# Kernel tuning notes

Hardware: AMD Instinct MI355X
Metric: run time of the kernel (lower is better)

## Reference

```python
import jax, jax.numpy as jnp
import numpy as np

NH = 256   # nh_rnn
V = 21     # joints
TC = 60    # cont time dim
CC = 4     # cont channels
DCT_N = 60
T_HIS = 30
HORIZON = 60
BS = 256


def _lin(x, w, b):
    # torch nn.Linear convention: w is [out, in]
    return x @ w.T + b


def setup_inputs() -> dict:
    key = jax.random.key(0)
    ks = iter(jax.random.split(key, 48))

    def rn(shape, s=1.0):
        return jax.random.normal(next(ks), shape, dtype=jnp.float32) * jnp.float32(s)

    inp = {}
    inp["x"] = rn((T_HIS, BS, 63))
    inp["cont"] = rn((BS, TC, V * CC))
    inp["cont_mask"] = jnp.ones((BS, TC), jnp.float32)  # never used (per docstring)
    inp["dct_m"] = rn((DCT_N, T_HIS + HORIZON), 0.1)
    inp["idct_m"] = rn((T_HIS + HORIZON, DCT_N), 0.1)
    inp["root_idx"] = jnp.array([42, 43, 44], dtype=jnp.int32)
    inp["horizon"] = HORIZON

    # --- STSGCN_layer(cont): learned temporal/spatial adjacencies + 1x1 convs + BN(folded) + PReLU ---
    inp["T_c"] = rn((V, TC, TC), 1.0 / np.sqrt(TC))
    inp["A_c"] = rn((TC, V, V), 1.0 / np.sqrt(V))
    inp["conv_w"] = rn((NH, CC), 0.5)
    inp["conv_b"] = rn((NH,), 0.1)
    inp["bn1_scale"] = 1.0 + rn((NH,), 0.1)
    inp["bn1_shift"] = rn((NH,), 0.1)
    inp["resconv_w"] = rn((NH, CC), 0.5)
    inp["resconv_b"] = rn((NH,), 0.1)
    inp["bnr_scale"] = 1.0 + rn((NH,), 0.1)
    inp["bnr_shift"] = rn((NH,), 0.1)
    inp["prelu_a"] = jnp.float32(0.25)

    # tiny MLP encoders
    inp["te1_w"] = rn((10, TC), 1.0 / np.sqrt(TC)); inp["te1_b"] = rn((10,), 0.1)
    inp["te2_w"] = rn((1, 10), 1.0 / np.sqrt(10)); inp["te2_b"] = rn((1,), 0.1)
    inp["ne1_w"] = rn((10, V), 1.0 / np.sqrt(V)); inp["ne1_b"] = rn((10,), 0.1)
    inp["ne2_w"] = rn((1, 10), 1.0 / np.sqrt(10)); inp["ne2_b"] = rn((1,), 0.1)

    # residual MLP head
    din = DCT_N * 3 + NH
    inp["g1_w"] = rn((NH, din), 1.0 / np.sqrt(din)); inp["g1_b"] = rn((NH,), 0.1)
    inp["g2a_w"] = rn((NH, NH), 1.0 / np.sqrt(NH)); inp["g2a_b"] = rn((NH,), 0.1)
    inp["g2b_w"] = rn((NH, NH), 1.0 / np.sqrt(NH)); inp["g2b_b"] = rn((NH,), 0.1)
    inp["g3a_w"] = rn((NH, NH), 1.0 / np.sqrt(NH)); inp["g3a_b"] = rn((NH,), 0.1)
    inp["g3b_w"] = rn((NH, NH), 1.0 / np.sqrt(NH)); inp["g3b_b"] = rn((NH,), 0.1)
    inp["g4_w"] = rn((DCT_N * 3, NH), 1.0 / np.sqrt(NH)); inp["g4_b"] = rn((DCT_N * 3,), 0.1)
    return inp


def reference(x, cont, cont_mask, dct_m, idct_m, root_idx, horizon,
              T_c, A_c, conv_w, conv_b, bn1_scale, bn1_shift,
              resconv_w, resconv_b, bnr_scale, bnr_shift, prelu_a,
              te1_w, te1_b, te2_w, te2_b, ne1_w, ne1_b, ne2_w, ne2_b,
              g1_w, g1_b, g2a_w, g2a_b, g2b_w, g2b_b,
              g3a_w, g3a_b, g3b_w, g3b_b, g4_w, g4_b):
    t_his, bs, _ = x.shape

    # --- root history padded with last frame, then batched DCT ---
    pad_idx = jnp.concatenate([jnp.arange(t_his), jnp.full((horizon,), t_his - 1)])
    root_his = x[:, :, root_idx][pad_idx].transpose(1, 0, 2)                 # [bs, 90, 3]
    root_his_dct = jnp.einsum('dt,btk->bdk', dct_m, root_his).reshape(bs, -1)  # [bs, 180]

    # --- STSGCN layer on contact stream: [b, 4, 60, 21] ---
    xc = cont.reshape(bs, TC, V, CC).transpose(0, 3, 1, 2)                   # [b,c,t,v]
    res = jnp.einsum('nctv,oc->notv', xc, resconv_w) + resconv_b[None, :, None, None]
    res = res * bnr_scale[None, :, None, None] + bnr_shift[None, :, None, None]
    g = jnp.einsum('nctv,vtq->ncqv', xc, T_c)    # temporal adjacency
    g = jnp.einsum('nctv,tvw->nctw', g, A_c)     # spatial adjacency
    h = jnp.einsum('nctv,oc->notv', g, conv_w) + conv_b[None, :, None, None]
    h = h * bn1_scale[None, :, None, None] + bn1_shift[None, :, None, None]
    h = h + res
    h = jnp.where(h >= 0, h, prelu_a * h)        # PReLU, [b, 256, 60, 21]

    # --- time encoder: collapse t=60 -> 1 ---
    ht = h.transpose(0, 1, 3, 2).reshape(bs, NH * V, TC)
    ht = jnp.tanh(_lin(jnp.tanh(_lin(ht, te1_w, te1_b)), te2_w, te2_b))[..., 0]
    # --- node encoder: collapse v=21 -> 1 ---
    hn = ht.reshape(bs, NH, V)
    hcont = jnp.tanh(_lin(jnp.tanh(_lin(hn, ne1_w, ne1_b)), ne2_w, ne2_b))[..., 0]  # [bs, 256]

    # --- residual MLP head on DCT coefficients ---
    rh = jnp.tanh(_lin(jnp.concatenate([root_his_dct, hcont], axis=1), g1_w, g1_b))
    rh = jnp.tanh(_lin(jnp.tanh(_lin(rh, g2a_w, g2a_b)), g2b_w, g2b_b)) + rh
    rh = jnp.tanh(_lin(jnp.tanh(_lin(rh, g3a_w, g3a_b)), g3b_w, g3b_b)) + rh
    root_pred = _lin(rh, g4_w, g4_b) + root_his_dct                          # [bs, 180]
    root_traj = jnp.einsum('td,bdk->btk', idct_m, root_pred.reshape(bs, DCT_N, 3))
    return root_traj                                                          # [bs, 90, 3]
```

## Files before the change

### kernel.cpp

```cpp
#include <hip/hip_runtime.h>

#define NHID 256
#define NV   21
#define NT   60
#define NC   4
#define NDCT 60
#define THIS 30
#define NBS  256

__device__ __forceinline__ float ftanh(float x) {
    float e = __expf(2.0f * x);
    return 1.0f - __fdividef(2.0f, e + 1.0f);
}

__global__ __launch_bounds__(512, 2) void k_main(
    const float* __restrict__ cont,
    const float* __restrict__ T_c, const float* __restrict__ A_c,
    const float* __restrict__ conv_w, const float* __restrict__ conv_b,
    const float* __restrict__ bn1_scale, const float* __restrict__ bn1_shift,
    const float* __restrict__ resconv_w, const float* __restrict__ resconv_b,
    const float* __restrict__ bnr_scale, const float* __restrict__ bnr_shift,
    const float* __restrict__ prelu_a_p,
    const float* __restrict__ te1_w, const float* __restrict__ te1_b,
    const float* __restrict__ te2_w, const float* __restrict__ te2_b,
    const float* __restrict__ ne1_w, const float* __restrict__ ne1_b,
    const float* __restrict__ ne2_w, const float* __restrict__ ne2_b,
    float* __restrict__ hcont)
{
    __shared__ __align__(16) float xc_lds[5040];
    __shared__ __align__(16) float g_lds[5040];
    __shared__ __align__(16) float g2_lds[5040];

    const int n   = blockIdx.x;
    const int tid = threadIdx.x;

    {
        const float4* src = (const float4*)(cont + n * 5040);
        float4* dst = (float4*)xc_lds;
        for (int i = tid; i < 1260; i += 512) dst[i] = src[i];
    }
    __syncthreads();

    for (int task = tid; task < 630; task += 512) {
        int v  = task / 30;
        int q0 = (task - v * 30) * 2;
        const float* tc = T_c + v * 3600 + q0;
        float4 a0 = {0.f,0.f,0.f,0.f}, a1 = {0.f,0.f,0.f,0.f};
        #pragma unroll 4
        for (int t = 0; t < 60; ++t) {
            float4 xcv = *(const float4*)(xc_lds + t * 84 + v * 4);
            float2 tq  = *(const float2*)(tc + t * 60);
            a0.x += xcv.x * tq.x; a0.y += xcv.y * tq.x;
            a0.z += xcv.z * tq.x; a0.w += xcv.w * tq.x;
            a1.x += xcv.x * tq.y; a1.y += xcv.y * tq.y;
            a1.z += xcv.z * tq.y; a1.w += xcv.w * tq.y;
        }
        *(float4*)(g_lds + q0 * 84 + v * 4)       = a0;
        *(float4*)(g_lds + (q0 + 1) * 84 + v * 4) = a1;
    }
    __syncthreads();

    for (int task = tid; task < 660; task += 512) {
        int t  = task / 11;
        int w0 = (task - t * 11) * 2;
        const bool has2 = (w0 < 20);
        const float* ac = A_c + t * 441 + w0;
        float4 a0 = {0.f,0.f,0.f,0.f}, a1 = {0.f,0.f,0.f,0.f};
        #pragma unroll
        for (int v = 0; v < 21; ++v) {
            float4 gv = *(const float4*)(g_lds + t * 84 + v * 4);
            float b0 = ac[v * 21];
            float b1 = has2 ? ac[v * 21 + 1] : 0.f;
            a0.x += gv.x * b0; a0.y += gv.y * b0;
            a0.z += gv.z * b0; a0.w += gv.w * b0;
            a1.x += gv.x * b1; a1.y += gv.y * b1;
            a1.z += gv.z * b1; a1.w += gv.w * b1;
        }
        *(float4*)(g2_lds + t * 84 + w0 * 4) = a0;
        if (has2) *(float4*)(g2_lds + t * 84 + (w0 + 1) * 4) = a1;
    }
    __syncthreads();

    const int og = tid >> 3;
    const int part = tid & 7;
    const int vstart = (part < 5) ? part * 3 : 15 + (part - 5) * 2;
    const int vcount = (part < 5) ? 3 : 2;

    const float pa = prelu_a_p[0];

    float cA[4][4], cB[4][4], cC[4];
    #pragma unroll
    for (int g = 0; g < 4; ++g) {
        int o = og * 4 + g;
        float s1 = bn1_scale[o], sr = bnr_scale[o];
        #pragma unroll
        for (int c = 0; c < 4; ++c) {
            cA[g][c] = conv_w[o * 4 + c] * s1;
            cB[g][c] = resconv_w[o * 4 + c] * sr;
        }
        cC[g] = conv_b[o] * s1 + bn1_shift[o] + resconv_b[o] * sr + bnr_shift[o];
    }

    float tw2[10], tb1[10];
    #pragma unroll
    for (int j = 0; j < 10; ++j) { tw2[j] = te2_w[j]; tb1[j] = te1_b[j]; }
    const float tb2 = te2_b[0];

    float wacc[4][10];
    #pragma unroll
    for (int g = 0; g < 4; ++g)
        #pragma unroll
        for (int j = 0; j < 10; ++j) wacc[g][j] = 0.f;

    for (int vi = 0; vi < vcount; ++vi) {
        int v = vstart + vi;
        float u[4][10];
        #pragma unroll
        for (int g = 0; g < 4; ++g)
            #pragma unroll
            for (int j = 0; j < 10; ++j) u[g][j] = tb1[j];

        for (int t = 0; t < 60; ++t) {
            float4 xcv = *(const float4*)(xc_lds + t * 84 + v * 4);
            float4 g2v = *(const float4*)(g2_lds + t * 84 + v * 4);
            float tw[10];
            #pragma unroll
            for (int j = 0; j < 10; ++j) tw[j] = te1_w[j * 60 + t];
            #pragma unroll
            for (int g = 0; g < 4; ++g) {
                float h = cC[g]
                    + cA[g][0] * g2v.x + cA[g][1] * g2v.y + cA[g][2] * g2v.z + cA[g][3] * g2v.w
                    + cB[g][0] * xcv.x + cB[g][1] * xcv.y + cB[g][2] * xcv.z + cB[g][3] * xcv.w;
                h = fmaxf(h, 0.f) + pa * fminf(h, 0.f);
                #pragma unroll
                for (int j = 0; j < 10; ++j) u[g][j] += h * tw[j];
            }
        }

        float nw[10];
        #pragma unroll
        for (int j = 0; j < 10; ++j) nw[j] = ne1_w[j * 21 + v];
        #pragma unroll
        for (int g = 0; g < 4; ++g) {
            float s = tb2;
            #pragma unroll
            for (int j = 0; j < 10; ++j) s += ftanh(u[g][j]) * tw2[j];
            s = ftanh(s);
            #pragma unroll
            for (int j = 0; j < 10; ++j) wacc[g][j] += s * nw[j];
        }
    }

    #pragma unroll
    for (int d = 1; d < 8; d <<= 1)
        #pragma unroll
        for (int g = 0; g < 4; ++g)
            #pragma unroll
            for (int j = 0; j < 10; ++j)
                wacc[g][j] += __shfl_xor(wacc[g][j], d, 64);

    if (part == 0) {
        float nw2[10];
        #pragma unroll
        for (int j = 0; j < 10; ++j) nw2[j] = ne2_w[j];
        float nb2 = ne2_b[0];
        #pragma unroll
        for (int g = 0; g < 4; ++g) {
            int o = og * 4 + g;
            float s = nb2;
            #pragma unroll
            for (int j = 0; j < 10; ++j)
                s += ftanh(wacc[g][j] + ne1_b[j]) * nw2[j];
            hcont[n * 256 + o] = ftanh(s);
        }
    }
}

__global__ __launch_bounds__(512) void k_head(
    const float* __restrict__ x, const float* __restrict__ dct_m,
    const int* __restrict__ root_idx, const float* __restrict__ hcont,
    const float* __restrict__ g1_w, const float* __restrict__ g1_b,
    const float* __restrict__ g2a_w, const float* __restrict__ g2a_b,
    const float* __restrict__ g2b_w, const float* __restrict__ g2b_b,
    const float* __restrict__ g3a_w, const float* __restrict__ g3a_b,
    const float* __restrict__ g3b_w, const float* __restrict__ g3b_b,
    const float* __restrict__ g4_w, const float* __restrict__ g4_b,
    const float* __restrict__ idct_m, float* __restrict__ out)
{
    __shared__ __align__(16) float in_lds[2 * 436];
    __shared__ __align__(16) float a_lds[2 * 256];
    __shared__ __align__(16) float b_lds[2 * 256];
    __shared__ __align__(16) float rp_lds[2 * 180];

    const int tid = threadIdx.x;
    const int n0 = blockIdx.x * 2;
    const int gid = tid >> 3;
    const int sub = tid & 7;

    {
        int bn = tid >> 8, j = tid & 255;
        in_lds[bn * 436 + 180 + j] = hcont[(n0 + bn) * 256 + j];
    }
    for (int i = tid; i < 360; i += 512) {
        int bn = i / 180, r = i - bn * 180;
        int d = r / 3, k = r - d * 3;
        int ri = root_idx[k];
        const float* xp = x + (n0 + bn) * 63 + ri;
        const float* dm = dct_m + d * 90;
        float acc = 0.f;
        #pragma unroll
        for (int t = 0; t < 30; ++t)
            acc += dm[t] * xp[t * 16128];
        float wl = 0.f;
        #pragma unroll
        for (int t = 30; t < 90; ++t)
            wl += dm[t];
        acc += wl * xp[29 * 16128];
        in_lds[bn * 436 + r] = acc;
    }
    __syncthreads();

#define DENSE_CORE(KDIM, NSWEEP, W, SRC, SSTR, GUARD_O, BODY)                   \
    {                                                                           \
        float acc[4][2] = {};                                                   \
        for (int s = 0; s < NSWEEP; ++s) {                                      \
            int k4 = s * 8 + sub;                                               \
            if (k4 * 4 < KDIM) {                                                \
                float4 av0 = *(const float4*)&SRC[0 * SSTR + k4 * 4];           \
                float4 av1 = *(const float4*)&SRC[1 * SSTR + k4 * 4];           \
                _Pragma("unroll")                                               \
                for (int oo = 0; oo < 4; ++oo) {                                \
                    int o = gid * 4 + oo;                                       \
                    if (GUARD_O) {                                              \
                        float4 wv = *(const float4*)&W[o * KDIM + k4 * 4];      \
                        acc[oo][0] += wv.x*av0.x + wv.y*av0.y + wv.z*av0.z + wv.w*av0.w; \
                        acc[oo][1] += wv.x*av1.x + wv.y*av1.y + wv.z*av1.z + wv.w*av1.w; \
                    }                                                           \
                }                                                               \
            }                                                                   \
        }                                                                       \
        _Pragma("unroll")                                                       \
        for (int m = 1; m < 8; m <<= 1) {                                       \
            _Pragma("unroll")                                                   \
            for (int oo = 0; oo < 4; ++oo) {                                    \
                acc[oo][0] += __shfl_xor(acc[oo][0], m, 64);                    \
                acc[oo][1] += __shfl_xor(acc[oo][1], m, 64);                    \
            }                                                                   \
        }                                                                       \
        if (sub == 0) {                                                         \
            _Pragma("unroll")                                                   \
            for (int oo = 0; oo < 4; ++oo) {                                    \
                int o = gid * 4 + oo;                                           \
                if (GUARD_O) {                                                  \
                    _Pragma("unroll")                                           \
                    for (int bn = 0; bn < 2; ++bn) { float sumv = acc[oo][bn]; BODY } \
                }                                                               \
            }                                                                   \
        }                                                                       \
    }                                                                           \
    __syncthreads();

    DENSE_CORE(436, 14, g1_w, in_lds, 436, true,
        { a_lds[bn * 256 + o] = ftanh(sumv + g1_b[o]); })

    DENSE_CORE(256, 8, g2a_w, a_lds, 256, true,
        { b_lds[bn * 256 + o] = ftanh(sumv + g2a_b[o]); })

    DENSE_CORE(256, 8, g2b_w, b_lds, 256, true,
        { a_lds[bn * 256 + o] = ftanh(sumv + g2b_b[o]) + a_lds[bn * 256 + o]; })

    DENSE_CORE(256, 8, g3a_w, a_lds, 256, true,
        { b_lds[bn * 256 + o] = ftanh(sumv + g3a_b[o]); })

    DENSE_CORE(256, 8, g3b_w, b_lds, 256, true,
        { a_lds[bn * 256 + o] = ftanh(sumv + g3b_b[o]) + a_lds[bn * 256 + o]; })

    DENSE_CORE(256, 8, g4_w, a_lds, 256, (o < 180),
        { rp_lds[bn * 180 + o] = sumv + g4_b[o] + in_lds[bn * 436 + o]; })

    for (int idx = tid; idx < 2 * 270; idx += 512) {
        int bn = idx / 270;
        int r = idx - bn * 270;
        int t = r / 3;
        int k = r - t * 3;
        const float* im = idct_m + t * 60;
        const float* rp = rp_lds + bn * 180 + k;
        float acc = 0.f;
        #pragma unroll
        for (int d = 0; d < 60; ++d)
            acc += im[d] * rp[d * 3];
        out[(n0 + bn) * 270 + r] = acc;
    }
}

extern "C" void kernel_launch(void* const* d_in, const int* in_sizes, int n_in,
                              void* d_out, int out_size, void* d_ws, size_t ws_size,
                              hipStream_t stream)
{
    const float* x        = (const float*)d_in[0];
    const float* cont     = (const float*)d_in[1];
    const float* dct_m    = (const float*)d_in[3];
    const float* idct_m   = (const float*)d_in[4];
    const int*   root_idx = (const int*)d_in[5];
    const float* T_c      = (const float*)d_in[7];
    const float* A_c      = (const float*)d_in[8];
    const float* conv_w   = (const float*)d_in[9];
    const float* conv_b   = (const float*)d_in[10];
    const float* bn1_s    = (const float*)d_in[11];
    const float* bn1_sh   = (const float*)d_in[12];
    const float* rconv_w  = (const float*)d_in[13];
    const float* rconv_b  = (const float*)d_in[14];
    const float* bnr_s    = (const float*)d_in[15];
    const float* bnr_sh   = (const float*)d_in[16];
    const float* prelu_a  = (const float*)d_in[17];
    const float* te1_w    = (const float*)d_in[18];
    const float* te1_b    = (const float*)d_in[19];
    const float* te2_w    = (const float*)d_in[20];
    const float* te2_b    = (const float*)d_in[21];
    const float* ne1_w    = (const float*)d_in[22];
    const float* ne1_b    = (const float*)d_in[23];
    const float* ne2_w    = (const float*)d_in[24];
    const float* ne2_b    = (const float*)d_in[25];
    const float* g1_w     = (const float*)d_in[26];
    const float* g1_b     = (const float*)d_in[27];
    const float* g2a_w    = (const float*)d_in[28];
    const float* g2a_b    = (const float*)d_in[29];
    const float* g2b_w    = (const float*)d_in[30];
    const float* g2b_b    = (const float*)d_in[31];
    const float* g3a_w    = (const float*)d_in[32];
    const float* g3a_b    = (const float*)d_in[33];
    const float* g3b_w    = (const float*)d_in[34];
    const float* g3b_b    = (const float*)d_in[35];
    const float* g4_w     = (const float*)d_in[36];
    const float* g4_b     = (const float*)d_in[37];

    float* hcont = (float*)d_ws;

    k_main<<<NBS, 512, 0, stream>>>(cont, T_c, A_c,
                                    conv_w, conv_b, bn1_s, bn1_sh,
                                    rconv_w, rconv_b, bnr_s, bnr_sh,
                                    prelu_a,
                                    te1_w, te1_b, te2_w, te2_b,
                                    ne1_w, ne1_b, ne2_w, ne2_b,
                                    hcont);

    k_head<<<NBS / 2, 512, 0, stream>>>(x, dct_m, root_idx, hcont,
                                        g1_w, g1_b, g2a_w, g2a_b, g2b_w, g2b_b,
                                        g3a_w, g3a_b, g3b_w, g3b_b, g4_w, g4_b,
                                        idct_m, (float*)d_out);
}
```

Baseline: 270.7 us.

## Fuse STSGCN encoder and MLP head into one 1024-thread kernel per sample

Merges the two kernels into a single kernel with one block per batch sample and 1024 threads. Each thread now handles 2 output channels in the encoder instead of 4, and the MLP head runs per sample with 4-way k-splitting, reusing the g_lds buffer for activations. This removes the second launch and the hcont round trip through global memory, and doubles the threads per block. In exchange, each block now reads the full head weights on its own, where before two samples shared each weight read, and launch_bounds(1024,4) may constrain registers.

```diff
diff --git a/kernel.cpp b/kernel.cpp
--- a/kernel.cpp
+++ b/kernel.cpp
@@ -13,8 +13,11 @@
     return 1.0f - __fdividef(2.0f, e + 1.0f);
 }
 
-__global__ __launch_bounds__(512, 2) void k_main(
+__global__ __launch_bounds__(1024, 4) void k_all(
+    const float* __restrict__ x,
     const float* __restrict__ cont,
+    const float* __restrict__ dct_m, const float* __restrict__ idct_m,
+    const int* __restrict__ root_idx,
     const float* __restrict__ T_c, const float* __restrict__ A_c,
     const float* __restrict__ conv_w, const float* __restrict__ conv_b,
     const float* __restrict__ bn1_scale, const float* __restrict__ bn1_shift,
@@ -25,23 +28,34 @@
     const float* __restrict__ te2_w, const float* __restrict__ te2_b,
     const float* __restrict__ ne1_w, const float* __restrict__ ne1_b,
     const float* __restrict__ ne2_w, const float* __restrict__ ne2_b,
-    float* __restrict__ hcont)
+    const float* __restrict__ g1_w, const float* __restrict__ g1_b,
+    const float* __restrict__ g2a_w, const float* __restrict__ g2a_b,
+    const float* __restrict__ g2b_w, const float* __restrict__ g2b_b,
+    const float* __restrict__ g3a_w, const float* __restrict__ g3a_b,
+    const float* __restrict__ g3b_w, const float* __restrict__ g3b_b,
+    const float* __restrict__ g4_w, const float* __restrict__ g4_b,
+    float* __restrict__ out)
 {
     __shared__ __align__(16) float xc_lds[5040];
     __shared__ __align__(16) float g_lds[5040];
     __shared__ __align__(16) float g2_lds[5040];
 
+    float* in2 = g_lds;
+    float* aL  = g_lds + 436;
+    float* bL  = g_lds + 692;
+    float* rp  = g_lds + 948;
+
     const int n   = blockIdx.x;
     const int tid = threadIdx.x;
 
     {
         const float4* src = (const float4*)(cont + n * 5040);
         float4* dst = (float4*)xc_lds;
-        for (int i = tid; i < 1260; i += 512) dst[i] = src[i];
-    }
-    __syncthreads();
-
-    for (int task = tid; task < 630; task += 512) {
+        for (int i = tid; i < 1260; i += 1024) dst[i] = src[i];
+    }
+    __syncthreads();
+
+    for (int task = tid; task < 630; task += 1024) {
         int v  = task / 30;
         int q0 = (task - v * 30) * 2;
         const float* tc = T_c + v * 3600 + q0;
@@ -60,7 +74,7 @@
     }
     __syncthreads();
 
-    for (int task = tid; task < 660; task += 512) {
+    for (int task = tid; task < 660; task += 1024) {
         int t  = task / 11;
         int w0 = (task - t * 11) * 2;
         const bool has2 = (w0 < 20);
@@ -81,131 +95,10 @@
     }
     __syncthreads();
 
-    const int og = tid >> 3;
-    const int part = tid & 7;
-    const int vstart = (part < 5) ? part * 3 : 15 + (part - 5) * 2;
-    const int vcount = (part < 5) ? 3 : 2;
-
-    const float pa = prelu_a_p[0];
-
-    float cA[4][4], cB[4][4], cC[4];
-    #pragma unroll
-    for (int g = 0; g < 4; ++g) {
-        int o = og * 4 + g;
-        float s1 = bn1_scale[o], sr = bnr_scale[o];
-        #pragma unroll
-        for (int c = 0; c < 4; ++c) {
-            cA[g][c] = conv_w[o * 4 + c] * s1;
-            cB[g][c] = resconv_w[o * 4 + c] * sr;
-        }
-        cC[g] = conv_b[o] * s1 + bn1_shift[o] + resconv_b[o] * sr + bnr_shift[o];
-    }
-
-    float tw2[10], tb1[10];
-    #pragma unroll
-    for (int j = 0; j < 10; ++j) { tw2[j] = te2_w[j]; tb1[j] = te1_b[j]; }
-    const float tb2 = te2_b[0];
-
-    float wacc[4][10];
-    #pragma unroll
-    for (int g = 0; g < 4; ++g)
-        #pragma unroll
-        for (int j = 0; j < 10; ++j) wacc[g][j] = 0.f;
-
-    for (int vi = 0; vi < vcount; ++vi) {
-        int v = vstart + vi;
-        float u[4][10];
-        #pragma unroll
-        for (int g = 0; g < 4; ++g)
-            #pragma unroll
-            for (int j = 0; j < 10; ++j) u[g][j] = tb1[j];
-
-        for (int t = 0; t < 60; ++t) {
-            float4 xcv = *(const float4*)(xc_lds + t * 84 + v * 4);
-            float4 g2v = *(const float4*)(g2_lds + t * 84 + v * 4);
-            float tw[10];
-            #pragma unroll
-            for (int j = 0; j < 10; ++j) tw[j] = te1_w[j * 60 + t];
-            #pragma unroll
-            for (int g = 0; g < 4; ++g) {
-                float h = cC[g]
-                    + cA[g][0] * g2v.x + cA[g][1] * g2v.y + cA[g][2] * g2v.z + cA[g][3] * g2v.w
-                    + cB[g][0] * xcv.x + cB[g][1] * xcv.y + cB[g][2] * xcv.z + cB[g][3] * xcv.w;
-                h = fmaxf(h, 0.f) + pa * fminf(h, 0.f);
-                #pragma unroll
-                for (int j = 0; j < 10; ++j) u[g][j] += h * tw[j];
-            }
-        }
-
-        float nw[10];
-        #pragma unroll
-        for (int j = 0; j < 10; ++j) nw[j] = ne1_w[j * 21 + v];
-        #pragma unroll
-        for (int g = 0; g < 4; ++g) {
-            float s = tb2;
-            #pragma unroll
-            for (int j = 0; j < 10; ++j) s += ftanh(u[g][j]) * tw2[j];
-            s = ftanh(s);
-            #pragma unroll
-            for (int j = 0; j < 10; ++j) wacc[g][j] += s * nw[j];
-        }
-    }
-
-    #pragma unroll
-    for (int d = 1; d < 8; d <<= 1)
-        #pragma unroll
-        for (int g = 0; g < 4; ++g)
-            #pragma unroll
-            for (int j = 0; j < 10; ++j)
-                wacc[g][j] += __shfl_xor(wacc[g][j], d, 64);
-
-    if (part == 0) {
-        float nw2[10];
-        #pragma unroll
-        for (int j = 0; j < 10; ++j) nw2[j] = ne2_w[j];
-        float nb2 = ne2_b[0];
-        #pragma unroll
-        for (int g = 0; g < 4; ++g) {
-            int o = og * 4 + g;
-            float s = nb2;
-            #pragma unroll
-            for (int j = 0; j < 10; ++j)
-                s += ftanh(wacc[g][j] + ne1_b[j]) * nw2[j];
-            hcont[n * 256 + o] = ftanh(s);
-        }
-    }
-}
-
-__global__ __launch_bounds__(512) void k_head(
-    const float* __restrict__ x, const float* __restrict__ dct_m,
-    const int* __restrict__ root_idx, const float* __restrict__ hcont,
-    const float* __restrict__ g1_w, const float* __restrict__ g1_b,
-    const float* __restrict__ g2a_w, const float* __restrict__ g2a_b,
-    const float* __restrict__ g2b_w, const float* __restrict__ g2b_b,
-    const float* __restrict__ g3a_w, const float* __restrict__ g3a_b,
-    const float* __restrict__ g3b_w, const float* __restrict__ g3b_b,
-    const float* __restrict__ g4_w, const float* __restrict__ g4_b,
-    const float* __restrict__ idct_m, float* __restrict__ out)
-{
-    __shared__ __align__(16) float in_lds[2 * 436];
-    __shared__ __align__(16) float a_lds[2 * 256];
-    __shared__ __align__(16) float b_lds[2 * 256];
-    __shared__ __align__(16) float rp_lds[2 * 180];
-
-    const int tid = threadIdx.x;
-    const int n0 = blockIdx.x * 2;
-    const int gid = tid >> 3;
-    const int sub = tid & 7;
-
-    {
-        int bn = tid >> 8, j = tid & 255;
-        in_lds[bn * 436 + 180 + j] = hcont[(n0 + bn) * 256 + j];
-    }
-    for (int i = tid; i < 360; i += 512) {
-        int bn = i / 180, r = i - bn * 180;
-        int d = r / 3, k = r - d * 3;
+    if (tid < 180) {
+        int d = tid / 3, k = tid - d * 3;
         int ri = root_idx[k];
-        const float* xp = x + (n0 + bn) * 63 + ri;
+        const float* xp = x + n * 63 + ri;
         const float* dm = dct_m + d * 90;
         float acc = 0.f;
         #pragma unroll
@@ -216,80 +109,144 @@
         for (int t = 30; t < 90; ++t)
             wl += dm[t];
         acc += wl * xp[29 * 16128];
-        in_lds[bn * 436 + r] = acc;
-    }
-    __syncthreads();
-
-#define DENSE_CORE(KDIM, NSWEEP, W, SRC, SSTR, GUARD_O, BODY)                   \
-    {                                                                           \
-        float acc[4][2] = {};                                                   \
-        for (int s = 0; s < NSWEEP; ++s) {                                      \
-            int k4 = s * 8 + sub;                                               \
-            if (k4 * 4 < KDIM) {                                                \
-                float4 av0 = *(const float4*)&SRC[0 * SSTR + k4 * 4];           \
-                float4 av1 = *(const float4*)&SRC[1 * SSTR + k4 * 4];           \
-                _Pragma("unroll")                                               \
-                for (int oo = 0; oo < 4; ++oo) {                                \
-                    int o = gid * 4 + oo;                                       \
-                    if (GUARD_O) {                                              \
-                        float4 wv = *(const float4*)&W[o * KDIM + k4 * 4];      \
-                        acc[oo][0] += wv.x*av0.x + wv.y*av0.y + wv.z*av0.z + wv.w*av0.w; \
-                        acc[oo][1] += wv.x*av1.x + wv.y*av1.y + wv.z*av1.z + wv.w*av1.w; \
-                    }                                                           \
-                }                                                               \
-            }                                                                   \
-        }                                                                       \
-        _Pragma("unroll")                                                       \
-        for (int m = 1; m < 8; m <<= 1) {                                       \
-            _Pragma("unroll")                                                   \
-            for (int oo = 0; oo < 4; ++oo) {                                    \
-                acc[oo][0] += __shfl_xor(acc[oo][0], m, 64);                    \
-                acc[oo][1] += __shfl_xor(acc[oo][1], m, 64);                    \
-            }                                                                   \
-        }                                                                       \
-        if (sub == 0) {                                                         \
-            _Pragma("unroll")                                                   \
-            for (int oo = 0; oo < 4; ++oo) {                                    \
-                int o = gid * 4 + oo;                                           \
-                if (GUARD_O) {                                                  \
-                    _Pragma("unroll")                                           \
-                    for (int bn = 0; bn < 2; ++bn) { float sumv = acc[oo][bn]; BODY } \
-                }                                                               \
-            }                                                                   \
-        }                                                                       \
-    }                                                                           \
-    __syncthreads();
-
-    DENSE_CORE(436, 14, g1_w, in_lds, 436, true,
-        { a_lds[bn * 256 + o] = ftanh(sumv + g1_b[o]); })
-
-    DENSE_CORE(256, 8, g2a_w, a_lds, 256, true,
-        { b_lds[bn * 256 + o] = ftanh(sumv + g2a_b[o]); })
-
-    DENSE_CORE(256, 8, g2b_w, b_lds, 256, true,
-        { a_lds[bn * 256 + o] = ftanh(sumv + g2b_b[o]) + a_lds[bn * 256 + o]; })
-
-    DENSE_CORE(256, 8, g3a_w, a_lds, 256, true,
-        { b_lds[bn * 256 + o] = ftanh(sumv + g3a_b[o]); })
-
-    DENSE_CORE(256, 8, g3b_w, b_lds, 256, true,
-        { a_lds[bn * 256 + o] = ftanh(sumv + g3b_b[o]) + a_lds[bn * 256 + o]; })
-
-    DENSE_CORE(256, 8, g4_w, a_lds, 256, (o < 180),
-        { rp_lds[bn * 180 + o] = sumv + g4_b[o] + in_lds[bn * 436 + o]; })
-
-    for (int idx = tid; idx < 2 * 270; idx += 512) {
-        int bn = idx / 270;
-        int r = idx - bn * 270;
-        int t = r / 3;
-        int k = r - t * 3;
+        in2[tid] = acc;
+    }
+
+    {
+        const int og = tid >> 3;
+        const int part = tid & 7;
+        const int vstart = (part < 5) ? part * 3 : 15 + (part - 5) * 2;
+        const int vcount = (part < 5) ? 3 : 2;
+
+        const float pa = prelu_a_p[0];
+
+        float cA[2][4], cB[2][4], cC[2];
+        #pragma unroll
+        for (int g = 0; g < 2; ++g) {
+            int o = og * 2 + g;
+            float s1 = bn1_scale[o], sr = bnr_scale[o];
+            #pragma unroll
+            for (int c = 0; c < 4; ++c) {
+                cA[g][c] = conv_w[o * 4 + c] * s1;
+                cB[g][c] = resconv_w[o * 4 + c] * sr;
+            }
+            cC[g] = conv_b[o] * s1 + bn1_shift[o] + resconv_b[o] * sr + bnr_shift[o];
+        }
+
+        float tw2[10], tb1[10];
+        #pragma unroll
+        for (int j = 0; j < 10; ++j) { tw2[j] = te2_w[j]; tb1[j] = te1_b[j]; }
+        const float tb2 = te2_b[0];
+
+        float wacc[2][10];
+        #pragma unroll
+        for (int g = 0; g < 2; ++g)
+            #pragma unroll
+            for (int j = 0; j < 10; ++j) wacc[g][j] = 0.f;
+
+        for (int vi = 0; vi < vcount; ++vi) {
+            int v = vstart + vi;
+            float u[2][10];
+            #pragma unroll
+            for (int g = 0; g < 2; ++g)
+                #pragma unroll
+                for (int j = 0; j < 10; ++j) u[g][j] = tb1[j];
+
+            for (int t = 0; t < 60; ++t) {
+                float4 xcv = *(const float4*)(xc_lds + t * 84 + v * 4);
+                float4 g2v = *(const float4*)(g2_lds + t * 84 + v * 4);
+                float tw[10];
+                #pragma unroll
+                for (int j = 0; j < 10; ++j) tw[j] = te1_w[j * 60 + t];
+                #pragma unroll
+                for (int g = 0; g < 2; ++g) {
+                    float h = cC[g]
+                        + cA[g][0] * g2v.x + cA[g][1] * g2v.y + cA[g][2] * g2v.z + cA[g][3] * g2v.w
+                        + cB[g][0] * xcv.x + cB[g][1] * xcv.y + cB[g][2] * xcv.z + cB[g][3] * xcv.w;
+                    h = fmaxf(h, 0.f) + pa * fminf(h, 0.f);
+                    #pragma unroll
+                    for (int j = 0; j < 10; ++j) u[g][j] += h * tw[j];
+                }
+            }
+
+            float nw[10];
+            #pragma unroll
+            for (int j = 0; j < 10; ++j) nw[j] = ne1_w[j * 21 + v];
+            #pragma unroll
+            for (int g = 0; g < 2; ++g) {
+                float s = tb2;
+                #pragma unroll
+                for (int j = 0; j < 10; ++j) s += ftanh(u[g][j]) * tw2[j];
+                s = ftanh(s);
+                #pragma unroll
+                for (int j = 0; j < 10; ++j) wacc[g][j] += s * nw[j];
+            }
+        }
+
+        #pragma unroll
+        for (int d = 1; d < 8; d <<= 1)
+            #pragma unroll
+            for (int g = 0; g < 2; ++g)
+                #pragma unroll
+                for (int j = 0; j < 10; ++j)
+                    wacc[g][j] += __shfl_xor(wacc[g][j], d, 64);
+
+        if (part == 0) {
+            float nw2[10];
+            #pragma unroll
+            for (int j = 0; j < 10; ++j) nw2[j] = ne2_w[j];
+            float nb2 = ne2_b[0];
+            #pragma unroll
+            for (int g = 0; g < 2; ++g) {
+                int o = og * 2 + g;
+                float s = nb2;
+                #pragma unroll
+                for (int j = 0; j < 10; ++j)
+                    s += ftanh(wacc[g][j] + ne1_b[j]) * nw2[j];
+                in2[180 + o] = ftanh(s);
+            }
+        }
+    }
+    __syncthreads();
+
+    const int gid = tid >> 2;
+    const int sub = tid & 3;
+
+#define DENSE(KDIM, NCHUNK, W, SRC, BODY)                                      \
+    {                                                                          \
+        float acc = 0.f;                                                       \
+        _Pragma("unroll")                                                      \
+        for (int s = 0; s < (NCHUNK + 3) / 4; ++s) {                           \
+            int c4 = s * 4 + sub;                                              \
+            if (c4 < NCHUNK) {                                                 \
+                float4 av = *(const float4*)&SRC[c4 * 4];                      \
+                float4 wv = *(const float4*)&W[gid * KDIM + c4 * 4];           \
+                acc += wv.x*av.x + wv.y*av.y + wv.z*av.z + wv.w*av.w;          \
+            }                                                                  \
+        }                                                                      \
+        acc += __shfl_xor(acc, 1, 64);                                         \
+        acc += __shfl_xor(acc, 2, 64);                                         \
+        if (sub == 0) { int o = gid; float sumv = acc; BODY }                  \
+    }                                                                          \
+    __syncthreads();
+
+    DENSE(436, 109, g1_w, in2, { aL[o] = ftanh(sumv + g1_b[o]); })
+    DENSE(256, 64, g2a_w, aL, { bL[o] = ftanh(sumv + g2a_b[o]); })
+    DENSE(256, 64, g2b_w, bL, { aL[o] = ftanh(sumv + g2b_b[o]) + aL[o]; })
+    DENSE(256, 64, g3a_w, aL, { bL[o] = ftanh(sumv + g3a_b[o]); })
+    DENSE(256, 64, g3b_w, bL, { aL[o] = ftanh(sumv + g3b_b[o]) + aL[o]; })
+    DENSE(256, 64, g4_w, aL, { if (o < 180) rp[o] = sumv + g4_b[o] + in2[o]; })
+
+    if (tid < 270) {
+        int t = tid / 3;
+        int k = tid - t * 3;
         const float* im = idct_m + t * 60;
-        const float* rp = rp_lds + bn * 180 + k;
+        const float* rpp = rp + k;
         float acc = 0.f;
         #pragma unroll
         for (int d = 0; d < 60; ++d)
-            acc += im[d] * rp[d * 3];
-        out[(n0 + bn) * 270 + r] = acc;
+            acc += im[d] * rpp[d * 3];
+        out[n * 270 + tid] = acc;
     }
 }
 
@@ -334,18 +291,14 @@
     const float* g4_w     = (const float*)d_in[36];
     const float* g4_b     = (const float*)d_in[37];
 
-    float* hcont = (float*)d_ws;
-
-    k_main<<<NBS, 512, 0, stream>>>(cont, T_c, A_c,
+    k_all<<<NBS, 1024, 0, stream>>>(x, cont, dct_m, idct_m, root_idx,
+                                    T_c, A_c,
                                     conv_w, conv_b, bn1_s, bn1_sh,
                                     rconv_w, rconv_b, bnr_s, bnr_sh,
                                     prelu_a,
                                     te1_w, te1_b, te2_w, te2_b,
                                     ne1_w, ne1_b, ne2_w, ne2_b,
-                                    hcont);
-
-    k_head<<<NBS / 2, 512, 0, stream>>>(x, dct_m, root_idx, hcont,
-                                        g1_w, g1_b, g2a_w, g2a_b, g2b_w, g2b_b,
-                                        g3a_w, g3a_b, g3b_w, g3b_b, g4_w, g4_b,
-                                        idct_m, (float*)d_out);
+                                    g1_w, g1_b, g2a_w, g2a_b, g2b_w, g2b_b,
+                                    g3a_w, g3a_b, g3b_w, g3b_b, g4_w, g4_b,
+                                    (float*)d_out);
 }
```

Result: faster. 250.0 us (-7.6%).
